# Performance work log

Hardware: AMD Instinct MI355X
Metric: run time of the kernel (lower is better)

The kernel has to match this reference:

```python
import jax, jax.numpy as jnp
import numpy as np

C = 2.0          # Poincare ball curvature (NCModel self.c = 2.0)
EPS = 1e-6
BN_EPS = 1e-5
SH_N, SS_N, HH_N, D, B, KG = 1195, 390, 805, 32, 32768, 27


def _expmap0(u):
    sc = jnp.sqrt(C)
    n = jnp.maximum(jnp.linalg.norm(u, axis=-1, keepdims=True), EPS)
    return jnp.tanh(sc * n) * u / (sc * n)


def _logmap0(p):
    sc = jnp.sqrt(C)
    n = jnp.maximum(jnp.linalg.norm(p, axis=-1, keepdims=True), EPS)
    s = jnp.minimum(sc * n, 1.0 - 1e-5)
    return jnp.arctanh(s) * p / (sc * n)


def _encode(x, adj, W, b):
    # hyperbolic GCN layer: map to ball, linear+aggregate in tangent space at origin
    t = _logmap0(_expmap0(x))
    t = jax.nn.relu(adj @ (t @ W + b))
    return _expmap0(t)


def _decode(h, adj, W, b):
    return adj @ (_logmap0(h) @ W + b)


def _bn(x, g, b):
    # BatchNorm1d in training mode (batch statistics, biased variance)
    m = jnp.mean(x, axis=0)
    v = jnp.mean((x - m) ** 2, axis=0)
    return (x - m) * jax.lax.rsqrt(v + BN_EPS) * g + b


def setup_inputs():
    key = jax.random.key(0)
    ks = iter(jax.random.split(key, 64))
    nk = lambda: next(ks)

    def lin(din, dout):
        s = 1.0 / np.sqrt(din)
        W = jax.random.uniform(nk(), (din, dout), minval=-s, maxval=s, dtype=jnp.float32)
        b = jax.random.uniform(nk(), (dout,), minval=-s, maxval=s, dtype=jnp.float32)
        return W, b

    inp = {}
    inp['x_SH'] = jax.random.randint(nk(), (SH_N,), 0, SH_N)
    inp['Spare_SH'] = jax.random.uniform(nk(), (SH_N, SH_N), dtype=jnp.float32) / SH_N
    inp['x_SS'] = jax.random.randint(nk(), (SS_N,), 0, SS_N)
    inp['Spare_SS'] = jax.random.uniform(nk(), (SS_N, SS_N), dtype=jnp.float32) / SS_N
    inp['x_HH'] = jax.random.randint(nk(), (HH_N,), 0, HH_N)
    inp['Spare_HH'] = jax.random.uniform(nk(), (HH_N, HH_N), dtype=jnp.float32) / HH_N
    inp['prescription'] = jax.random.uniform(nk(), (B, SS_N), dtype=jnp.float32)
    inp['kgOneHot'] = jax.random.uniform(nk(), (HH_N, KG), dtype=jnp.float32)
    # embedding tables (note: HH_embedding is Embedding(sh_num, d) in the source)
    inp['emb_SH'] = jax.random.normal(nk(), (SH_N, D), dtype=jnp.float32)
    inp['emb_SS'] = jax.random.normal(nk(), (SS_N, D), dtype=jnp.float32)
    inp['emb_HH'] = jax.random.normal(nk(), (SH_N, D), dtype=jnp.float32)
    for tag in ['sh', 'sh2', 'ss', 'hh']:
        We, be = lin(D, D)
        Wd, bd = lin(D, D)
        inp['We_' + tag], inp['be_' + tag] = We, be
        inp['Wd_' + tag], inp['bd_' + tag] = Wd, bd
    inp['W_shems'], inp['b_shems'] = lin(D, D)
    inp['W_mlp1'], inp['b_mlp1'] = lin(D, D)
    inp['g_bn1'], inp['bb_bn1'] = jnp.ones((D,), jnp.float32), jnp.zeros((D,), jnp.float32)
    inp['W_cs'], inp['b_cs'] = lin(2 * D, D)
    inp['W_ch'], inp['b_ch'] = lin(2 * D, D)
    inp['W_L'], inp['b_L'] = lin(D + KG, D)
    inp['W_mlp'], inp['b_mlp'] = lin(D, D)
    inp['g_si'], inp['bb_si'] = jnp.ones((D,), jnp.float32), jnp.zeros((D,), jnp.float32)
    return inp


def reference(x_SH, Spare_SH, x_SS, Spare_SS, x_HH, Spare_HH, prescription, kgOneHot,
              emb_SH, emb_SS, emb_HH,
              We_sh, be_sh, Wd_sh, bd_sh,
              We_sh2, be_sh2, Wd_sh2, bd_sh2,
              We_ss, be_ss, Wd_ss, bd_ss,
              We_hh, be_hh, Wd_hh, bd_hh,
              W_shems, b_shems, W_mlp1, b_mlp1, g_bn1, bb_bn1,
              W_cs, b_cs, W_ch, b_ch, W_L, b_L, W_mlp, b_mlp, g_si, bb_si):
    x_SH1 = emb_SH[x_SH]                                                  # [1195, 32]
    x_SH2 = _decode(_encode(x_SH1, Spare_SH, We_sh, be_sh), Spare_SH, Wd_sh, bd_sh)
    x_SH5 = _decode(_encode(x_SH2, Spare_SH, We_sh2, be_sh2), Spare_SH, Wd_sh2, bd_sh2)
    x_SH3 = x_SH1 @ W_shems + b_shems
    x = (x_SH2 + x_SH3 + x_SH5) / 3.0
    x = jnp.tanh(_bn(x @ W_mlp1 + b_mlp1, g_bn1, bb_bn1))                 # [1195, 32]

    x_ss2 = _decode(_encode(emb_SS[x_SS], Spare_SS, We_ss, be_ss), Spare_SS, Wd_ss, bd_ss)
    x_hh2 = _decode(_encode(emb_HH[x_HH], Spare_HH, We_hh, be_hh), Spare_HH, Wd_hh, bd_hh)
    x_hh2 = jnp.concatenate([x_hh2, kgOneHot], axis=-1) @ W_L + b_L      # [805, 32]

    es = jnp.concatenate([x[:SS_N], x_ss2], axis=1) @ W_cs + b_cs        # [390, 32]
    eh = jnp.concatenate([x[SS_N:], x_hh2], axis=1) @ W_ch + b_ch        # [805, 32]

    e_synd = prescription @ es                                           # [B, 32]
    e_synd = e_synd / jnp.sum(prescription, axis=1, keepdims=True)
    e_synd = jax.nn.relu(_bn(e_synd @ W_mlp + b_mlp, g_si, bb_si))
    return e_synd @ eh.T                                                 # [B, 805]
```

## Files before the change

kernel.cpp:

```cpp
#include <hip/hip_runtime.h>

#define KSPLIT 4


__device__ __forceinline__ float red32(float v){
  #pragma unroll
  for(int m=16;m;m>>=1) v += __shfl_xor(v, m, 32);
  return v;
}

__device__ __forceinline__ float logexp_rt(float x){
  const float sc = 1.4142135623730951f;
  float n  = sqrtf(red32(x*x));
  float n1 = fmaxf(n, 1e-6f);
  float a  = sc*n1;
  float p  = tanhf(a)/a * x;
  float np = sqrtf(red32(p*p));
  float np1= fmaxf(np, 1e-6f);
  float s  = fminf(sc*np1, 1.0f - 1e-5f);
  float at = 0.5f*logf((1.f+s)/(1.f-s));
  return at/(sc*np1) * p;
}

__device__ __forceinline__ float matvec32(float tv, const float* __restrict__ W,
                                          const float* __restrict__ bb, int j){
  float acc = bb[j];
  #pragma unroll
  for(int k=0;k<32;k++) acc = fmaf(__shfl(tv, k, 32), W[k*32+j], acc);
  return acc;
}

__device__ __forceinline__ float psum4(const float* __restrict__ P, int N, int idx){
  int s = N*32;
  return P[idx] + P[s+idx] + P[2*s+idx] + P[3*s+idx];
}


__global__ __launch_bounds__(256) void k_prep(
    const int* __restrict__ xsh, const int* __restrict__ xss, const int* __restrict__ xhh,
    const float* __restrict__ embSH, const float* __restrict__ embSS, const float* __restrict__ embHH,
    const float* __restrict__ We_sh, const float* __restrict__ be_sh,
    const float* __restrict__ We_ss, const float* __restrict__ be_ss,
    const float* __restrict__ We_hh, const float* __restrict__ be_hh,
    float* __restrict__ x1sh, float* __restrict__ ush,
    float* __restrict__ uss, float* __restrict__ uhh)
{
  int t = threadIdx.x, j = t&31;
  int g = blockIdx.x*8 + (t>>5);
  if(g >= 2390) return;
  const int* xi; const float* emb; const float* We; const float* be; float* uo; int r;
  float* x1o = nullptr;
  if(g < 1195){ r=g;      xi=xsh; emb=embSH; We=We_sh; be=be_sh; uo=ush; x1o=x1sh; }
  else if(g < 1585){ r=g-1195; xi=xss; emb=embSS; We=We_ss; be=be_ss; uo=uss; }
  else {            r=g-1585; xi=xhh; emb=embHH; We=We_hh; be=be_hh; uo=uhh; }
  float x = emb[xi[r]*32 + j];
  if(x1o) x1o[r*32+j] = x;
  float tv = logexp_rt(x);
  uo[r*32+j] = matvec32(tv, We, be, j);
}

struct AdjCfg { const float* S; const float* X; float* P; int N; int nrb; };

__global__ __launch_bounds__(256) void k_adj(AdjCfg c0, AdjCfg c1, AdjCfg c2, int e0, int e1)
{
  __shared__ float Xl[64][33];
  int b = blockIdx.x;
  AdjCfg c; int local;
  if(b < e0){ c = c0; local = b; }
  else if(b < e1){ c = c1; local = b - e0; }
  else { c = c2; local = b - e1; }
  int ks = local / c.nrb, rb = local % c.nrb;
  int N = c.N;
  int klen = (N + KSPLIT - 1)/KSPLIT;
  int kbeg = ks*klen, kend = min(kbeg+klen, N);
  int t = threadIdx.x, j = t&31, hw = t>>5;
  int r0 = rb*16;
  int ra = r0 + hw, rbv = r0 + hw + 8;
  bool va = ra < N, vb = rbv < N;
  const float* __restrict__ Sa = c.S + (long)(va? ra : 0) * N;
  const float* __restrict__ Sb = c.S + (long)(vb? rbv: 0) * N;
  float acc0 = 0.f, acc1 = 0.f;
  for(int k0 = kbeg; k0 < kend; k0 += 64){
    int kc = min(64, kend - k0);
    __syncthreads();
    #pragma unroll
    for(int q=0;q<8;q++){
      int e = t + 256*q; int kr = e>>5, jj = e&31;
      Xl[kr][jj] = (kr < kc) ? c.X[(k0+kr)*32 + jj] : 0.f;
    }
    __syncthreads();
    if(kc == 64){
      #pragma unroll 16
      for(int k=0;k<64;k++){
        float x = Xl[k][j];
        acc0 = fmaf(Sa[k0+k], x, acc0);
        acc1 = fmaf(Sb[k0+k], x, acc1);
      }
    } else {
      for(int k=0;k<kc;k++){
        float x = Xl[k][j];
        acc0 = fmaf(Sa[k0+k], x, acc0);
        acc1 = fmaf(Sb[k0+k], x, acc1);
      }
    }
  }
  float* P = c.P + (long)ks * N * 32;
  if(va) P[ra *32 + j] = acc0;
  if(vb) P[rbv*32 + j] = acc1;
}

__global__ __launch_bounds__(256) void k_pw1(
    const float* __restrict__ pvsh, const float* __restrict__ pvss, const float* __restrict__ pvhh,
    const float* __restrict__ Wd_sh, const float* __restrict__ bd_sh,
    const float* __restrict__ Wd_ss, const float* __restrict__ bd_ss,
    const float* __restrict__ Wd_hh, const float* __restrict__ bd_hh,
    float* __restrict__ wsh, float* __restrict__ wss, float* __restrict__ whh)
{
  int t=threadIdx.x, j=t&31;
  int g = blockIdx.x*8 + (t>>5);
  if(g>=2390) return;
  const float* P; const float* Wd; const float* bd; float* w; int r, N;
  if(g<1195){ r=g;      N=1195; P=pvsh; Wd=Wd_sh; bd=bd_sh; w=wsh; }
  else if(g<1585){ r=g-1195; N=390; P=pvss; Wd=Wd_ss; bd=bd_ss; w=wss; }
  else {          r=g-1585; N=805; P=pvhh; Wd=Wd_hh; bd=bd_hh; w=whh; }
  float v = psum4(P, N, r*32+j);
  float tv = logexp_rt(fmaxf(v, 0.f));
  w[r*32+j] = matvec32(tv, Wd, bd, j);
}

__global__ __launch_bounds__(256) void k_pw2(
    const float* __restrict__ pxsh, const float* __restrict__ pxss, const float* __restrict__ pxhh,
    const float* __restrict__ We2, const float* __restrict__ be2,
    const float* __restrict__ kg, const float* __restrict__ W_L, const float* __restrict__ b_L,
    float* __restrict__ x2, float* __restrict__ u2,
    float* __restrict__ xss2, float* __restrict__ xhh2)
{
  int t=threadIdx.x, j=t&31;
  int g = blockIdx.x*8 + (t>>5);
  if(g>=2390) return;
  if(g < 1195){
    int r = g;
    float v = psum4(pxsh, 1195, r*32+j);
    x2[r*32+j] = v;
    u2[r*32+j] = matvec32(logexp_rt(v), We2, be2, j);
  } else if(g < 1585){
    int r = g-1195;
    xss2[r*32+j] = psum4(pxss, 390, r*32+j);
  } else {
    int r = g-1585;
    float v = psum4(pxhh, 805, r*32+j);
    float acc = b_L[j];
    #pragma unroll
    for(int k=0;k<32;k++) acc = fmaf(__shfl(v,k,32), W_L[k*32+j], acc);
    #pragma unroll
    for(int k=0;k<27;k++) acc = fmaf(kg[r*27+k], W_L[(32+k)*32+j], acc);
    xhh2[r*32+j] = acc;
  }
}

__global__ __launch_bounds__(256) void k_pwdec1(
    const float* __restrict__ P, int N,
    const float* __restrict__ Wd, const float* __restrict__ bd, float* __restrict__ w)
{
  int t=threadIdx.x, j=t&31;
  int r = blockIdx.x*8 + (t>>5);
  if(r>=N) return;
  float v = psum4(P, N, r*32+j);
  w[r*32+j] = matvec32(logexp_rt(fmaxf(v,0.f)), Wd, bd, j);
}

__global__ __launch_bounds__(256) void k_pw4(
    const float* __restrict__ px5, const float* __restrict__ x2, const float* __restrict__ x1,
    const float* __restrict__ Wsh, const float* __restrict__ bsh,
    const float* __restrict__ W1, const float* __restrict__ b1, float* __restrict__ y)
{
  int t=threadIdx.x, j=t&31;
  int r = blockIdx.x*8 + (t>>5);
  if(r>=1195) return;
  int idx = r*32+j;
  float x5 = psum4(px5, 1195, idx);
  float a  = matvec32(x1[idx], Wsh, bsh, j);
  float xv = (x2[idx] + x5 + a) / 3.0f;
  y[idx] = matvec32(xv, W1, b1, j);
}

__global__ __launch_bounds__(1024) void k_bn1(
    const float* __restrict__ y, const float* __restrict__ g, const float* __restrict__ b,
    float* __restrict__ scl, float* __restrict__ sft)
{
  __shared__ float r1[32][33];
  __shared__ float msh[32];
  int t=threadIdx.x; int j=t&31, rg=t>>5;
  float s1=0.f;
  for(int r=rg;r<1195;r+=32) s1 += y[r*32+j];
  r1[rg][j] = s1;
  __syncthreads();
  if(t<32){ float S=0.f; for(int q=0;q<32;q++) S += r1[q][t]; msh[t] = S/1195.f; }
  __syncthreads();
  float m = msh[j];
  float s2=0.f;
  for(int r=rg;r<1195;r+=32){ float d = y[r*32+j]-m; s2 += d*d; }
  __syncthreads();
  r1[rg][j] = s2;
  __syncthreads();
  if(t<32){
    float S=0.f; for(int q=0;q<32;q++) S += r1[q][t];
    float var = S/1195.f;
    float sc = g[t]*rsqrtf(var + 1e-5f);
    scl[t] = sc; sft[t] = b[t] - msh[t]*sc;
  }
}

__global__ __launch_bounds__(256) void k_eseh(
    const float* __restrict__ y, const float* __restrict__ scl1, const float* __restrict__ sft1,
    const float* __restrict__ xss2, const float* __restrict__ xhh2,
    const float* __restrict__ W_cs, const float* __restrict__ b_cs,
    const float* __restrict__ W_ch, const float* __restrict__ b_ch,
    float* __restrict__ es, float* __restrict__ eh)
{
  int t=threadIdx.x, j=t&31;
  int r = blockIdx.x*8 + (t>>5);
  if(r>=1195) return;
  float xr = tanhf(fmaf(y[r*32+j], scl1[j], sft1[j]));
  const float* W; const float* bb; const float* x2p; float* o;
  if(r < 390){ W=W_cs; bb=b_cs; x2p = xss2 + r*32;      o = es + r*32; }
  else       { W=W_ch; bb=b_ch; x2p = xhh2 + (r-390)*32; o = eh + (r-390)*32; }
  float c2 = x2p[j];
  float acc = bb[j];
  #pragma unroll
  for(int k=0;k<32;k++){
    acc = fmaf(__shfl(xr, k, 32), W[k*32+j],      acc);
    acc = fmaf(__shfl(c2, k, 32), W[(32+k)*32+j], acc);
  }
  o[j] = acc;
}


__global__ __launch_bounds__(256) void k_pgemm(
    const float* __restrict__ P, const float* __restrict__ es,
    const float* __restrict__ Wm, const float* __restrict__ bm,
    float* __restrict__ tout, double* __restrict__ stats)
{
  __shared__ __align__(16) float Pl[64][68];
  __shared__ float esl[64][33];
  __shared__ float red[2][8][33];
  int t = threadIdx.x, j = t&31, isub = t>>5;
  long i0 = (long)blockIdx.x * 64;
  float acc[8], ps[8];
  #pragma unroll
  for(int a=0;a<8;a++){ acc[a]=0.f; ps[a]=0.f; }
  for(int k0=0;k0<390;k0+=64){
    __syncthreads();
    #pragma unroll
    for(int q=0;q<8;q++){
      int row = isub + 8*q, c2 = j;
      int kk = k0 + 2*c2;
      float2 v = make_float2(0.f,0.f);
      if(kk < 390) v = *(const float2*)(P + (i0+row)*390 + kk);
      Pl[row][2*c2]   = v.x;
      Pl[row][2*c2+1] = v.y;
      ps[q] += v.x + v.y;
    }
    #pragma unroll
    for(int q=0;q<8;q++){
      int kr = isub + 8*q, jj = j;
      esl[kr][jj] = (k0+kr < 390) ? es[(k0+kr)*32 + jj] : 0.f;
    }
    __syncthreads();
    #pragma unroll
    for(int k4=0;k4<16;k4++){
      float4 pv[8];
      #pragma unroll
      for(int a=0;a<8;a++) pv[a] = *(const float4*)&Pl[isub+8*a][4*k4];
      #pragma unroll
      for(int kk=0;kk<4;kk++){
        float ev = esl[4*k4+kk][j];
        #pragma unroll
        for(int a=0;a<8;a++) acc[a] = fmaf(((const float*)&pv[a])[kk], ev, acc[a]);
      }
    }
  }
  float en[8];
  #pragma unroll
  for(int a=0;a<8;a++){
    float rs = red32(ps[a]);
    en[a] = acc[a] / rs;
  }
  float tm[8]; float bmj = bm[j];
  #pragma unroll
  for(int a=0;a<8;a++) tm[a] = bmj;
  for(int k=0;k<32;k++){
    float wv = Wm[k*32+j];
    #pragma unroll
    for(int a=0;a<8;a++) tm[a] = fmaf(__shfl(en[a], k, 32), wv, tm[a]);
  }
  float s1=0.f, s2=0.f;
  #pragma unroll
  for(int a=0;a<8;a++){
    tout[(i0 + isub + 8*a)*32 + j] = tm[a];
    s1 += tm[a]; s2 += tm[a]*tm[a];
  }
  red[0][isub][j] = s1; red[1][isub][j] = s2;
  __syncthreads();
  if(t < 32){
    float S1=0.f, S2=0.f;
    #pragma unroll
    for(int g2=0; g2<8; g2++){ S1 += red[0][g2][t]; S2 += red[1][g2][t]; }
    atomicAdd(&stats[t],    (double)S1);
    atomicAdd(&stats[32+t], (double)S2);
  }
}

__global__ __launch_bounds__(64) void k_bnfin(
    const double* __restrict__ stats, const float* __restrict__ g, const float* __restrict__ b,
    float* __restrict__ scl, float* __restrict__ sft)
{
  int j = threadIdx.x; if(j>=32) return;
  double mean = stats[j] * (1.0/32768.0);
  double var  = stats[32+j] * (1.0/32768.0) - mean*mean;
  float sc = g[j] * rsqrtf((float)var + 1e-5f);
  scl[j] = sc; sft[j] = b[j] - (float)mean*sc;
}

__global__ __launch_bounds__(256) void k_out(
    const float* __restrict__ tin, const float* __restrict__ eh,
    const float* __restrict__ scl, const float* __restrict__ sft,
    float* __restrict__ out)
{
  __shared__ __align__(16) float zt[4][32][36];
  __shared__ float el[32][68];
  int t = threadIdx.x;
  int w = t>>6, lane = t&63;
  long i0 = (long)(blockIdx.x & 255) * 128;
  int  j0 = (int)(blockIdx.x >> 8) * 64;
  int kf = t&31, ib = t>>5;
  float sc = scl[kf], sh = sft[kf];
  #pragma unroll
  for(int q=0;q<16;q++){
    int i = ib + 8*q;
    float v = tin[(i0+i)*32 + kf];
    v = fmaxf(fmaf(v, sc, sh), 0.f);
    zt[i&3][kf][i>>2] = v;
  }
  #pragma unroll
  for(int q=0;q<8;q++){
    int jr = ib + 8*q;
    int jg = j0 + jr;
    el[kf][jr] = (jg < 805) ? eh[(long)jg*32 + kf] : 0.f;
  }
  __syncthreads();
  float acc[32];
  #pragma unroll
  for(int a=0;a<32;a++) acc[a]=0.f;
  #pragma unroll 4
  for(int k=0;k<32;k++){
    float ev = el[k][lane];
    #pragma unroll
    for(int q4=0;q4<8;q4++){
      float4 zv = *(const float4*)&zt[w][k][4*q4];
      acc[4*q4+0] = fmaf(zv.x, ev, acc[4*q4+0]);
      acc[4*q4+1] = fmaf(zv.y, ev, acc[4*q4+1]);
      acc[4*q4+2] = fmaf(zv.z, ev, acc[4*q4+2]);
      acc[4*q4+3] = fmaf(zv.w, ev, acc[4*q4+3]);
    }
  }
  int jg = j0 + lane;
  if(jg < 805){
    #pragma unroll
    for(int ri=0;ri<32;ri++){
      long row = i0 + 4*ri + w;
      out[row*805 + jg] = acc[ri];
    }
  }
}


extern "C" void kernel_launch(void* const* d_in, const int* in_sizes, int n_in,
                              void* d_out, int out_size, void* d_ws, size_t ws_size,
                              hipStream_t stream)
{
  const int*   x_SH  = (const int*)  d_in[0];
  const float* S_SH  = (const float*)d_in[1];
  const int*   x_SS  = (const int*)  d_in[2];
  const float* S_SS  = (const float*)d_in[3];
  const int*   x_HH  = (const int*)  d_in[4];
  const float* S_HH  = (const float*)d_in[5];
  const float* presc = (const float*)d_in[6];
  const float* kg    = (const float*)d_in[7];
  const float* embSH = (const float*)d_in[8];
  const float* embSS = (const float*)d_in[9];
  const float* embHH = (const float*)d_in[10];
  const float* We_sh = (const float*)d_in[11]; const float* be_sh = (const float*)d_in[12];
  const float* Wd_sh = (const float*)d_in[13]; const float* bd_sh = (const float*)d_in[14];
  const float* We_sh2= (const float*)d_in[15]; const float* be_sh2= (const float*)d_in[16];
  const float* Wd_sh2= (const float*)d_in[17]; const float* bd_sh2= (const float*)d_in[18];
  const float* We_ss = (const float*)d_in[19]; const float* be_ss = (const float*)d_in[20];
  const float* Wd_ss = (const float*)d_in[21]; const float* bd_ss = (const float*)d_in[22];
  const float* We_hh = (const float*)d_in[23]; const float* be_hh = (const float*)d_in[24];
  const float* Wd_hh = (const float*)d_in[25]; const float* bd_hh = (const float*)d_in[26];
  const float* W_shems=(const float*)d_in[27]; const float* b_shems=(const float*)d_in[28];
  const float* W_mlp1= (const float*)d_in[29]; const float* b_mlp1= (const float*)d_in[30];
  const float* g_bn1 = (const float*)d_in[31]; const float* bb_bn1= (const float*)d_in[32];
  const float* W_cs  = (const float*)d_in[33]; const float* b_cs  = (const float*)d_in[34];
  const float* W_ch  = (const float*)d_in[35]; const float* b_ch  = (const float*)d_in[36];
  const float* W_L   = (const float*)d_in[37]; const float* b_L   = (const float*)d_in[38];
  const float* W_mlp = (const float*)d_in[39]; const float* b_mlp = (const float*)d_in[40];
  const float* g_si  = (const float*)d_in[41]; const float* bb_si = (const float*)d_in[42];
  float* outp = (float*)d_out;

  float* wsf = (float*)d_ws;
  size_t off = 0;
  auto alloc = [&](size_t n){ float* p = wsf + off; off += (n + 3) & ~(size_t)3; return p; };
  float* t_buf = alloc(32768UL*32);
  float* psh   = alloc(4UL*1195*32);
  float* pss   = alloc(4UL*390*32);
  float* phh   = alloc(4UL*805*32);
  float* x1    = alloc(1195*32);
  float* ush   = alloc(1195*32);
  float* wsh   = alloc(1195*32);
  float* x2    = alloc(1195*32);
  float* u2    = alloc(1195*32);
  float* w2    = alloc(1195*32);
  float* ybuf  = alloc(1195*32);
  float* uss   = alloc(390*32);
  float* wss_  = alloc(390*32);
  float* xss2  = alloc(390*32);
  float* uhh   = alloc(805*32);
  float* whh_  = alloc(805*32);
  float* xhh2  = alloc(805*32);
  float* esb   = alloc(390*32);
  float* ehb   = alloc(805*32);
  float* scl1  = alloc(32); float* sft1 = alloc(32);
  float* scl2  = alloc(32); float* sft2 = alloc(32);
  double* stats = (double*)(wsf + off); off += 128;

  k_prep<<<299,256,0,stream>>>(x_SH,x_SS,x_HH, embSH,embSS,embHH,
                               We_sh,be_sh, We_ss,be_ss, We_hh,be_hh,
                               x1, ush, uss, uhh);

  AdjCfg a0{S_SH, ush, psh, 1195, 75}, a1{S_SS, uss, pss, 390, 25}, a2{S_HH, uhh, phh, 805, 51};
  k_adj<<<604,256,0,stream>>>(a0,a1,a2, 300, 400);

  k_pw1<<<299,256,0,stream>>>(psh,pss,phh, Wd_sh,bd_sh, Wd_ss,bd_ss, Wd_hh,bd_hh,
                              wsh, wss_, whh_);

  AdjCfg b0{S_SH, wsh, psh, 1195, 75}, b1{S_SS, wss_, pss, 390, 25}, b2{S_HH, whh_, phh, 805, 51};
  k_adj<<<604,256,0,stream>>>(b0,b1,b2, 300, 400);

  k_pw2<<<299,256,0,stream>>>(psh,pss,phh, We_sh2,be_sh2, kg, W_L,b_L,
                              x2, u2, xss2, xhh2);

  AdjCfg c0{S_SH, u2, psh, 1195, 75};
  k_adj<<<300,256,0,stream>>>(c0,c0,c0, 300, 300);

  k_pwdec1<<<150,256,0,stream>>>(psh, 1195, Wd_sh2, bd_sh2, w2);

  AdjCfg d0{S_SH, w2, psh, 1195, 75};
  k_adj<<<300,256,0,stream>>>(d0,d0,d0, 300, 300);

  k_pw4<<<150,256,0,stream>>>(psh, x2, x1, W_shems,b_shems, W_mlp1,b_mlp1, ybuf);

  k_bn1<<<1,1024,0,stream>>>(ybuf, g_bn1, bb_bn1, scl1, sft1);

  k_eseh<<<150,256,0,stream>>>(ybuf, scl1, sft1, xss2, xhh2,
                               W_cs,b_cs, W_ch,b_ch, esb, ehb);

  hipMemsetAsync(stats, 0, 64*sizeof(double), stream);
  k_pgemm<<<512,256,0,stream>>>(presc, esb, W_mlp, b_mlp, t_buf, stats);
  k_bnfin<<<1,64,0,stream>>>(stats, g_si, bb_si, scl2, sft2);
  k_out<<<256*13,256,0,stream>>>(t_buf, ehb, scl2, sft2, outp);
}
```

Baseline: 446.7 us.

## Shrink pgemm row tile to 16 and replace double atomics with per-block partials

The prescription GEMM kernel now gives each block 16 rows instead of 64, which launches 2048 blocks instead of 512 and fills more compute units on the memory-bound read of the 32768x390 matrix. BatchNorm statistics are no longer accumulated with double-precision global atomics. Each block writes its own float partial sums, and a 1024-thread finalize kernel reduces them in double, which also removes the memset. In exchange the es tile is reloaded into shared memory four times as often, and the finalize kernel does more work.

```diff
diff --git a/kernel.cpp b/kernel.cpp
--- a/kernel.cpp
+++ b/kernel.cpp
@@ -239,64 +239,63 @@
 __global__ __launch_bounds__(256) void k_pgemm(
     const float* __restrict__ P, const float* __restrict__ es,
     const float* __restrict__ Wm, const float* __restrict__ bm,
-    float* __restrict__ tout, double* __restrict__ stats)
-{
-  __shared__ __align__(16) float Pl[64][68];
+    float* __restrict__ tout, float* __restrict__ partial)
+{
+  __shared__ __align__(16) float Pl[16][68];
   __shared__ float esl[64][33];
   __shared__ float red[2][8][33];
   int t = threadIdx.x, j = t&31, isub = t>>5;
-  long i0 = (long)blockIdx.x * 64;
-  float acc[8], ps[8];
-  #pragma unroll
-  for(int a=0;a<8;a++){ acc[a]=0.f; ps[a]=0.f; }
+  long i0 = (long)blockIdx.x * 16;
+  float acc[2], ps[2];
+  acc[0]=acc[1]=0.f; ps[0]=ps[1]=0.f;
   for(int k0=0;k0<390;k0+=64){
     __syncthreads();
     #pragma unroll
-    for(int q=0;q<8;q++){
-      int row = isub + 8*q, c2 = j;
-      int kk = k0 + 2*c2;
+    for(int q=0;q<2;q++){
+      int row = isub + 8*q;
+      int kk = k0 + 2*j;
       float2 v = make_float2(0.f,0.f);
       if(kk < 390) v = *(const float2*)(P + (i0+row)*390 + kk);
-      Pl[row][2*c2]   = v.x;
-      Pl[row][2*c2+1] = v.y;
+      Pl[row][2*j]   = v.x;
+      Pl[row][2*j+1] = v.y;
       ps[q] += v.x + v.y;
     }
     #pragma unroll
     for(int q=0;q<8;q++){
-      int kr = isub + 8*q, jj = j;
-      esl[kr][jj] = (k0+kr < 390) ? es[(k0+kr)*32 + jj] : 0.f;
+      int kr = isub + 8*q;
+      esl[kr][j] = (k0+kr < 390) ? es[(k0+kr)*32 + j] : 0.f;
     }
     __syncthreads();
     #pragma unroll
     for(int k4=0;k4<16;k4++){
-      float4 pv[8];
+      float4 pv[2];
       #pragma unroll
-      for(int a=0;a<8;a++) pv[a] = *(const float4*)&Pl[isub+8*a][4*k4];
+      for(int a=0;a<2;a++) pv[a] = *(const float4*)&Pl[isub+8*a][4*k4];
       #pragma unroll
       for(int kk=0;kk<4;kk++){
         float ev = esl[4*k4+kk][j];
         #pragma unroll
-        for(int a=0;a<8;a++) acc[a] = fmaf(((const float*)&pv[a])[kk], ev, acc[a]);
+        for(int a=0;a<2;a++) acc[a] = fmaf(((const float*)&pv[a])[kk], ev, acc[a]);
       }
     }
   }
-  float en[8];
-  #pragma unroll
-  for(int a=0;a<8;a++){
+  float en[2];
+  #pragma unroll
+  for(int a=0;a<2;a++){
     float rs = red32(ps[a]);
     en[a] = acc[a] / rs;
   }
-  float tm[8]; float bmj = bm[j];
-  #pragma unroll
-  for(int a=0;a<8;a++) tm[a] = bmj;
+  float tm[2]; float bmj = bm[j];
+  tm[0] = bmj; tm[1] = bmj;
+  #pragma unroll
   for(int k=0;k<32;k++){
     float wv = Wm[k*32+j];
-    #pragma unroll
-    for(int a=0;a<8;a++) tm[a] = fmaf(__shfl(en[a], k, 32), wv, tm[a]);
+    tm[0] = fmaf(__shfl(en[0], k, 32), wv, tm[0]);
+    tm[1] = fmaf(__shfl(en[1], k, 32), wv, tm[1]);
   }
   float s1=0.f, s2=0.f;
   #pragma unroll
-  for(int a=0;a<8;a++){
+  for(int a=0;a<2;a++){
     tout[(i0 + isub + 8*a)*32 + j] = tm[a];
     s1 += tm[a]; s2 += tm[a]*tm[a];
   }
@@ -306,20 +305,36 @@
     float S1=0.f, S2=0.f;
     #pragma unroll
     for(int g2=0; g2<8; g2++){ S1 += red[0][g2][t]; S2 += red[1][g2][t]; }
-    atomicAdd(&stats[t],    (double)S1);
-    atomicAdd(&stats[32+t], (double)S2);
-  }
-}
-
-__global__ __launch_bounds__(64) void k_bnfin(
-    const double* __restrict__ stats, const float* __restrict__ g, const float* __restrict__ b,
+    partial[(long)blockIdx.x*64 + t]      = S1;
+    partial[(long)blockIdx.x*64 + 32 + t] = S2;
+  }
+}
+
+__global__ __launch_bounds__(1024) void k_bnfin(
+    const float* __restrict__ partial, const float* __restrict__ g, const float* __restrict__ b,
     float* __restrict__ scl, float* __restrict__ sft)
 {
-  int j = threadIdx.x; if(j>=32) return;
-  double mean = stats[j] * (1.0/32768.0);
-  double var  = stats[32+j] * (1.0/32768.0) - mean*mean;
-  float sc = g[j] * rsqrtf((float)var + 1e-5f);
-  scl[j] = sc; sft[j] = b[j] - (float)mean*sc;
+  __shared__ double sh[16][64];
+  __shared__ double tot[64];
+  int t = threadIdx.x;
+  int col = t&63, grp = t>>6;
+  double s = 0.0;
+  for(int bb2 = grp; bb2 < 2048; bb2 += 16) s += (double)partial[(long)bb2*64 + col];
+  sh[grp][col] = s;
+  __syncthreads();
+  if(t < 64){
+    double S = 0.0;
+    #pragma unroll
+    for(int q=0;q<16;q++) S += sh[q][t];
+    tot[t] = S;
+  }
+  __syncthreads();
+  if(t < 32){
+    double mean = tot[t]      * (1.0/32768.0);
+    double var  = tot[32+t]   * (1.0/32768.0) - mean*mean;
+    float sc = g[t] * rsqrtf((float)var + 1e-5f);
+    scl[t] = sc; sft[t] = b[t] - (float)mean*sc;
+  }
 }
 
 __global__ __launch_bounds__(256) void k_out(
@@ -412,6 +427,7 @@
   size_t off = 0;
   auto alloc = [&](size_t n){ float* p = wsf + off; off += (n + 3) & ~(size_t)3; return p; };
   float* t_buf = alloc(32768UL*32);
+  float* part  = alloc(2048UL*64);
   float* psh   = alloc(4UL*1195*32);
   float* pss   = alloc(4UL*390*32);
   float* phh   = alloc(4UL*805*32);
@@ -432,7 +448,6 @@
   float* ehb   = alloc(805*32);
   float* scl1  = alloc(32); float* sft1 = alloc(32);
   float* scl2  = alloc(32); float* sft2 = alloc(32);
-  double* stats = (double*)(wsf + off); off += 128;
 
   k_prep<<<299,256,0,stream>>>(x_SH,x_SS,x_HH, embSH,embSS,embHH,
                                We_sh,be_sh, We_ss,be_ss, We_hh,be_hh,
@@ -465,8 +480,7 @@
   k_eseh<<<150,256,0,stream>>>(ybuf, scl1, sft1, xss2, xhh2,
                                W_cs,b_cs, W_ch,b_ch, esb, ehb);
 
-  hipMemsetAsync(stats, 0, 64*sizeof(double), stream);
-  k_pgemm<<<512,256,0,stream>>>(presc, esb, W_mlp, b_mlp, t_buf, stats);
-  k_bnfin<<<1,64,0,stream>>>(stats, g_si, bb_si, scl2, sft2);
+  k_pgemm<<<2048,256,0,stream>>>(presc, esb, W_mlp, b_mlp, t_buf, part);
+  k_bnfin<<<1,1024,0,stream>>>(part, g_si, bb_si, scl2, sft2);
   k_out<<<256*13,256,0,stream>>>(t_buf, ehb, scl2, sft2, outp);
 }
```

Result: no change. 453.5 us (+1.5%).
